# Performance work log

Hardware: AMD Instinct MI355X
Metric: run time of the kernel (lower is better)

The kernel has to match this reference:

```python
import jax, jax.numpy as jnp
import numpy as np

EPS = 1e-6

D_MODEL = 1024
D_STATE = 16
D_CONV = 4
BATCH = 2
SEQ = 2048
D_INNER = 2 * D_MODEL
DT_RANK = D_MODEL // 16
D_FF = 4 * D_MODEL


def rmsnorm(x, w):
    return x * w * jax.lax.rsqrt(jnp.mean(x * x, axis=-1, keepdims=True) + EPS)


def setup_inputs() -> dict:
    key = jax.random.key(0)
    ks = jax.random.split(key, 12)
    s = lambda k, shape, scale=0.02: (jax.random.normal(k, shape, jnp.float32) * scale)
    # S4D-real style A init: A_log[d, n] = log(n+1)
    A_log = jnp.log(jnp.broadcast_to(jnp.arange(1, D_STATE + 1, dtype=jnp.float32), (D_INNER, D_STATE)))
    return {
        "x": jax.random.normal(ks[0], (BATCH, SEQ, D_MODEL), jnp.float32),
        "norm1_w": jnp.ones((D_MODEL,), jnp.float32),
        "norm2_w": jnp.ones((D_MODEL,), jnp.float32),
        "in_proj_w": s(ks[1], (2 * D_INNER, D_MODEL)),
        "conv_w": s(ks[2], (D_INNER, 1, D_CONV), 0.2),
        "conv_b": jnp.zeros((D_INNER,), jnp.float32),
        "x_proj_w": s(ks[3], (DT_RANK + 2 * D_STATE, D_INNER)),
        "dt_proj_w": s(ks[4], (D_INNER, DT_RANK), 0.1),
        "dt_proj_b": jax.random.uniform(ks[5], (D_INNER,), jnp.float32, -4.0, -3.0),
        "A_log": A_log,
        "D": jnp.ones((D_INNER,), jnp.float32),
        "out_proj_w": s(ks[6], (D_MODEL, D_INNER)),
        "w1": s(ks[7], (D_FF, D_MODEL)),
        "w3": s(ks[8], (D_FF, D_MODEL)),
        "w2": s(ks[9], (D_MODEL, D_FF)),
    }


def _ssm(h, in_proj_w, conv_w, conv_b, x_proj_w, dt_proj_w, dt_proj_b, A_log, D, out_proj_w):
    d_inner, d_state = A_log.shape
    dt_rank = dt_proj_w.shape[1]
    d_conv = conv_w.shape[-1]
    bsz = h.shape[0]

    xz = jnp.einsum('bld,ed->ble', h, in_proj_w)          # (B, L, 2*d_inner)
    xin, z = jnp.split(xz, 2, axis=-1)

    # causal depthwise conv over time
    xc = jnp.swapaxes(xin, 1, 2)                           # (B, d_inner, L)
    xc = jax.lax.conv_general_dilated(xc, conv_w, (1,), [(d_conv - 1, 0)],
                                      feature_group_count=d_inner)
    xin = jax.nn.silu(jnp.swapaxes(xc + conv_b[:, None], 1, 2))  # (B, L, d_inner)

    x_dbl = jnp.einsum('bld,ed->ble', xin, x_proj_w)       # (B, L, dt_rank + 2*d_state)
    dt, Bm, Cm = jnp.split(x_dbl, [dt_rank, dt_rank + d_state], axis=-1)
    delta = jax.nn.softplus(jnp.einsum('blr,dr->bld', dt, dt_proj_w) + dt_proj_b)
    A = -jnp.exp(A_log)                                    # (d_inner, d_state)

    def step(hstate, t):
        delta_t, B_t, C_t, x_t = t                         # (B,d), (B,n), (B,n), (B,d)
        dA = jnp.exp(delta_t[..., None] * A)               # (B, d_inner, d_state)
        dBx = (delta_t * x_t)[..., None] * B_t[:, None, :]
        hstate = dA * hstate + dBx
        y = jnp.einsum('bdn,bn->bd', hstate, C_t)
        return hstate, y

    tm = lambda a: jnp.swapaxes(a, 0, 1)                   # time-major
    h0 = jnp.zeros((bsz, d_inner, d_state), h.dtype)
    _, ys = jax.lax.scan(step, h0, (tm(delta), tm(Bm), tm(Cm), tm(xin)))
    y = jnp.swapaxes(ys, 0, 1) + xin * D                   # (B, L, d_inner)
    return jnp.einsum('bld,ed->ble', y * jax.nn.silu(z), out_proj_w)


def reference(x, norm1_w, norm2_w, in_proj_w, conv_w, conv_b, x_proj_w,
              dt_proj_w, dt_proj_b, A_log, D, out_proj_w, w1, w3, w2):
    x = x + _ssm(rmsnorm(x, norm1_w), in_proj_w, conv_w, conv_b, x_proj_w,
                 dt_proj_w, dt_proj_b, A_log, D, out_proj_w)
    h = rmsnorm(x, norm2_w)
    mlp = jnp.einsum('blf,df->bld',
                     jax.nn.silu(jnp.einsum('bld,fd->blf', h, w1)) * jnp.einsum('bld,fd->blf', h, w3),
                     w2)
    return x + mlp
```

## Files before the change

kernel.cpp:

```cpp
#include <hip/hip_runtime.h>

#define DEV __device__ __forceinline__

typedef unsigned short u16;
typedef float f32x4 __attribute__((ext_vector_type(4)));
typedef __bf16 bf16x8 __attribute__((ext_vector_type(8)));

#define CHUNK 64
#define NCH 32

DEV u16 f2b(float f) {
    unsigned u = __builtin_bit_cast(unsigned, f);
    u += 0x7fffu + ((u >> 16) & 1u);
    return (u16)(u >> 16);
}
DEV float b2f(u16 h) { return __builtin_bit_cast(float, (unsigned)h << 16); }
DEV float silu_(float v) { return v / (1.f + __expf(-v)); }
DEV float b2f_lo(unsigned w) { return __builtin_bit_cast(float, w << 16); }
DEV float b2f_hi(unsigned w) { return __builtin_bit_cast(float, w & 0xffff0000u); }
DEV void unpack8(uint4 w, float* f) {
    f[0] = b2f_lo(w.x); f[1] = b2f_hi(w.x);
    f[2] = b2f_lo(w.y); f[3] = b2f_hi(w.y);
    f[4] = b2f_lo(w.z); f[5] = b2f_hi(w.z);
    f[6] = b2f_lo(w.w); f[7] = b2f_hi(w.w);
}

DEV void gload16(const void* g, void* l) {
    __builtin_amdgcn_global_load_lds((const __attribute__((address_space(1))) unsigned int*)g,
                                     (__attribute__((address_space(3))) unsigned int*)l,
                                     16, 0, 0);
}

__global__ __launch_bounds__(256) void cvt_bf16_k(const float* __restrict__ in,
                                                  u16* __restrict__ out, int n4) {
    int i = blockIdx.x * 256 + threadIdx.x;
    if (i >= n4) return;
    float4 v = reinterpret_cast<const float4*>(in)[i];
    ushort4 o;
    o.x = f2b(v.x); o.y = f2b(v.y); o.z = f2b(v.z); o.w = f2b(v.w);
    reinterpret_cast<ushort4*>(out)[i] = o;
}

__global__ __launch_bounds__(256) void rmsnorm_k(const float* __restrict__ x,
                                                 const float* __restrict__ w,
                                                 u16* __restrict__ out) {
    int row = blockIdx.x;
    int t = threadIdx.x;
    float4 v = reinterpret_cast<const float4*>(x + (size_t)row * 1024)[t];
    float s = v.x * v.x + v.y * v.y + v.z * v.z + v.w * v.w;
#pragma unroll
    for (int off = 32; off; off >>= 1) s += __shfl_xor(s, off);
    __shared__ float red[4];
    if ((t & 63) == 0) red[t >> 6] = s;
    __syncthreads();
    float tot = red[0] + red[1] + red[2] + red[3];
    float scale = rsqrtf(tot * (1.f / 1024.f) + 1e-6f);
    float4 wv = reinterpret_cast<const float4*>(w)[t];
    ushort4 o;
    o.x = f2b(v.x * wv.x * scale);
    o.y = f2b(v.y * wv.y * scale);
    o.z = f2b(v.z * wv.z * scale);
    o.w = f2b(v.w * wv.w * scale);
    reinterpret_cast<ushort4*>(out + (size_t)row * 1024)[t] = o;
}

template <int EPI>
__global__ __launch_bounds__(256) void gemm_bt(
    const u16* __restrict__ A, int lda,
    const u16* __restrict__ B, int ldb,
    void* C, int ldc,
    int N, int K,
    const float* __restrict__ bias,
    const void* aux, int ldaux) {
    __shared__ u16 lsA[128 * 32];
    __shared__ u16 lsB[128 * 32];
    const int t = threadIdx.x;
    const int l = t & 63, w = t >> 6;
    const int m0 = blockIdx.x * 128, n0 = blockIdx.y * 128;
    const int wm = w >> 1, wn = w & 1;
    const int lrow = l & 15, lk8 = (l >> 4) * 8;

    const int sr = w * 16 + (l >> 2);
    const int sc = (l & 3) * 8;
    const u16* gA0 = A + (size_t)(m0 + sr) * lda + sc;
    const u16* gA1 = gA0 + (size_t)64 * lda;
    int nr0 = n0 + sr;      if (nr0 > N - 1) nr0 = N - 1;
    int nr1 = n0 + 64 + sr; if (nr1 > N - 1) nr1 = N - 1;
    const u16* gB0 = B + (size_t)nr0 * ldb + sc;
    const u16* gB1 = B + (size_t)nr1 * ldb + sc;
    u16* ldsA0 = &lsA[w * 512];
    u16* ldsA1 = &lsA[2048 + w * 512];
    u16* ldsB0 = &lsB[w * 512];
    u16* ldsB1 = &lsB[2048 + w * 512];

    f32x4 acc[4][4];
#pragma unroll
    for (int i = 0; i < 4; ++i)
#pragma unroll
        for (int j = 0; j < 4; ++j) acc[i][j] = (f32x4){0.f, 0.f, 0.f, 0.f};

    for (int k0 = 0; k0 < K; k0 += 32) {
        gload16(gA0 + k0, ldsA0);
        gload16(gA1 + k0, ldsA1);
        gload16(gB0 + k0, ldsB0);
        gload16(gB1 + k0, ldsB1);
        __syncthreads();
        bf16x8 af[4], bfr[4];
#pragma unroll
        for (int i = 0; i < 4; ++i)
            af[i] = *reinterpret_cast<const bf16x8*>(&lsA[(wm * 64 + i * 16 + lrow) * 32 + lk8]);
#pragma unroll
        for (int j = 0; j < 4; ++j)
            bfr[j] = *reinterpret_cast<const bf16x8*>(&lsB[(wn * 64 + j * 16 + lrow) * 32 + lk8]);
#pragma unroll
        for (int i = 0; i < 4; ++i)
#pragma unroll
            for (int j = 0; j < 4; ++j)
                acc[i][j] = __builtin_amdgcn_mfma_f32_16x16x32_bf16(af[i], bfr[j], acc[i][j], 0, 0, 0);
        __syncthreads();
    }

    const int rbase = m0 + wm * 64 + (l >> 4) * 4;
    const int cbase = n0 + wn * 64 + (l & 15);
#pragma unroll
    for (int i = 0; i < 4; ++i) {
#pragma unroll
        for (int j = 0; j < 4; ++j) {
            int col = cbase + j * 16;
            if (col >= N) continue;
#pragma unroll
            for (int r = 0; r < 4; ++r) {
                int row = rbase + i * 16 + r;
                float v = acc[i][j][r];
                size_t idx = (size_t)row * ldc + col;
                if constexpr (EPI == 0) {
                    ((u16*)C)[idx] = f2b(v);
                } else if constexpr (EPI == 1) {
                    float z = v + bias[col];
                    float sp = z > 20.f ? z : log1pf(__expf(z));
                    ((u16*)C)[idx] = f2b(sp);
                } else if constexpr (EPI == 2) {
                    ((float*)C)[idx] = v + ((const float*)aux)[(size_t)row * ldaux + col];
                } else if constexpr (EPI == 4) {
                    float g = b2f(((const u16*)aux)[(size_t)row * ldaux + col]);
                    ((u16*)C)[idx] = f2b(silu_(g) * v);
                }
            }
        }
    }
}

__global__ __launch_bounds__(256) void conv_k(const u16* __restrict__ xraw,
                                              const float* __restrict__ cw,
                                              const float* __restrict__ cb,
                                              u16* __restrict__ xin) {
    size_t idx = (size_t)blockIdx.x * 256 + threadIdx.x;
    if (idx >= (size_t)4096 * 2048) return;
    int d = (int)(idx & 2047);
    int m = (int)(idx >> 11);
    int lpos = m & 2047, b = m >> 11;
    float acc = cb[d];
#pragma unroll
    for (int j = 0; j < 4; ++j) {
        int lj = lpos - 3 + j;
        if (lj >= 0)
            acc += b2f(xraw[((size_t)(b * 2048 + lj) << 11) + d]) * cw[d * 4 + j];
    }
    xin[idx] = f2b(silu_(acc));
}

__global__ __launch_bounds__(256) void scan_p1(const u16* __restrict__ dlt,
                                               const u16* __restrict__ xin,
                                               const u16* __restrict__ xdbl,
                                               const float* __restrict__ A_log,
                                               float* __restrict__ hfin,
                                               float* __restrict__ sdlt) {
    int blk = blockIdx.x;
    int g = blk & 7, c = (blk >> 3) & 31, b = blk >> 8;
    int d = g * 256 + threadIdx.x;
    __shared__ u16 bc[CHUNK * 32];
    {
        int i = threadIdx.x;
        int r = i >> 2, q = i & 3;
        const u16* src = xdbl + ((size_t)(b * 2048 + c * CHUNK + r) * 96 + 64 + q * 8);
        *reinterpret_cast<uint4*>(&bc[r * 32 + q * 8]) = *reinterpret_cast<const uint4*>(src);
    }
    __syncthreads();
    float A2[16];
#pragma unroll
    for (int n = 0; n < 16; ++n) A2[n] = -__expf(A_log[d * 16 + n]) * 1.44269504f;
    float h[16];
#pragma unroll
    for (int n = 0; n < 16; ++n) h[n] = 0.f;
    float S = 0.f;
    size_t base = ((size_t)(b * 2048 + c * CHUNK) << 11) + d;
#pragma unroll 4
    for (int t = 0; t < CHUNK; ++t) {
        float dl = b2f(dlt[base + ((size_t)t << 11)]);
        float xv = b2f(xin[base + ((size_t)t << 11)]);
        S += dl;
        float dx = dl * xv;
        float Bv[16];
        unpack8(*reinterpret_cast<const uint4*>(&bc[t * 32]), Bv);
        unpack8(*reinterpret_cast<const uint4*>(&bc[t * 32 + 8]), Bv + 8);
#pragma unroll
        for (int n = 0; n < 16; ++n)
            h[n] = __builtin_amdgcn_exp2f(dl * A2[n]) * h[n] + dx * Bv[n];
    }
    float* hf = hfin + ((size_t)((b * NCH + c) * 2048 + d) << 4);
#pragma unroll
    for (int n = 0; n < 4; ++n)
        reinterpret_cast<float4*>(hf)[n] = (float4){h[4*n], h[4*n+1], h[4*n+2], h[4*n+3]};
    sdlt[(b * NCH + c) * 2048 + d] = S;
}

__global__ __launch_bounds__(256) void scan_p2(const float* __restrict__ hfin,
                                               const float* __restrict__ sdlt,
                                               const float* __restrict__ A_log,
                                               float* __restrict__ hini) {
    int t = blockIdx.x * 256 + threadIdx.x;
    int n = t & 15, d = (t >> 4) & 2047, b = t >> 15;
    float A2 = -__expf(A_log[d * 16 + n]) * 1.44269504f;
    float h = 0.f;
    for (int c = 0; c < NCH; ++c) {
        size_t idx = ((size_t)((b * NCH + c) * 2048 + d) << 4) + n;
        hini[idx] = h;
        float P = __builtin_amdgcn_exp2f(A2 * sdlt[(b * NCH + c) * 2048 + d]);
        h = P * h + hfin[idx];
    }
}

__global__ __launch_bounds__(256) void scan_p3(const u16* __restrict__ dlt,
                                               const u16* __restrict__ xin,
                                               const u16* __restrict__ xdbl,
                                               const u16* __restrict__ zb,
                                               const float* __restrict__ A_log,
                                               const float* __restrict__ Dv,
                                               const float* __restrict__ hini,
                                               u16* __restrict__ y2) {
    int blk = blockIdx.x;
    int g = blk & 7, c = (blk >> 3) & 31, b = blk >> 8;
    int d = g * 256 + threadIdx.x;
    __shared__ u16 bc[CHUNK * 32];
    {
        int i = threadIdx.x;
        int r = i >> 2, q = i & 3;
        const u16* src = xdbl + ((size_t)(b * 2048 + c * CHUNK + r) * 96 + 64 + q * 8);
        *reinterpret_cast<uint4*>(&bc[r * 32 + q * 8]) = *reinterpret_cast<const uint4*>(src);
    }
    __syncthreads();
    float A2[16];
#pragma unroll
    for (int n = 0; n < 16; ++n) A2[n] = -__expf(A_log[d * 16 + n]) * 1.44269504f;
    float h[16];
    const float* hi = hini + ((size_t)((b * NCH + c) * 2048 + d) << 4);
#pragma unroll
    for (int n = 0; n < 4; ++n) {
        float4 v = reinterpret_cast<const float4*>(hi)[n];
        h[4*n] = v.x; h[4*n+1] = v.y; h[4*n+2] = v.z; h[4*n+3] = v.w;
    }
    float Dd = Dv[d];
    size_t base = ((size_t)(b * 2048 + c * CHUNK) << 11) + d;
#pragma unroll 4
    for (int t = 0; t < CHUNK; ++t) {
        float dl = b2f(dlt[base + ((size_t)t << 11)]);
        float xv = b2f(xin[base + ((size_t)t << 11)]);
        float zv = b2f(zb[base + ((size_t)t << 11)]);
        float dx = dl * xv;
        float Bv[16], Cv[16];
        unpack8(*reinterpret_cast<const uint4*>(&bc[t * 32]), Bv);
        unpack8(*reinterpret_cast<const uint4*>(&bc[t * 32 + 8]), Bv + 8);
        unpack8(*reinterpret_cast<const uint4*>(&bc[t * 32 + 16]), Cv);
        unpack8(*reinterpret_cast<const uint4*>(&bc[t * 32 + 24]), Cv + 8);
        float y = 0.f;
#pragma unroll
        for (int n = 0; n < 16; ++n) {
            h[n] = __builtin_amdgcn_exp2f(dl * A2[n]) * h[n] + dx * Bv[n];
            y += h[n] * Cv[n];
        }
        y = (y + xv * Dd) * silu_(zv);
        y2[base + ((size_t)t << 11)] = f2b(y);
    }
}


extern "C" void kernel_launch(void* const* d_in, const int* in_sizes, int n_in,
                              void* d_out, int out_size, void* d_ws, size_t ws_size,
                              hipStream_t stream) {
    const float* x         = (const float*)d_in[0];
    const float* n1w       = (const float*)d_in[1];
    const float* n2w       = (const float*)d_in[2];
    const float* w_inproj  = (const float*)d_in[3];
    const float* conv_w    = (const float*)d_in[4];
    const float* conv_b    = (const float*)d_in[5];
    const float* x_projw   = (const float*)d_in[6];
    const float* w_dtproj  = (const float*)d_in[7];
    const float* dt_b      = (const float*)d_in[8];
    const float* A_log     = (const float*)d_in[9];
    const float* Dv        = (const float*)d_in[10];
    const float* w_outproj = (const float*)d_in[11];
    const float* w1        = (const float*)d_in[12];
    const float* w3        = (const float*)d_in[13];
    const float* w2        = (const float*)d_in[14];

    char* ws = (char*)d_ws;
    u16* wbuf    = (u16*)(ws + 0);
    u16* h_bf    = (u16*)(ws + 8388608);
    u16* xraw_bf = (u16*)(ws + 16777216);
    u16* z_bf    = (u16*)(ws + 33554432);
    u16* xin_bf  = (u16*)(ws + 50331648);
    u16* dlt_bf  = (u16*)(ws + 67108864);
    u16* xdbl_bf = (u16*)(ws + 83886080);
    float* sdlt  = (float*)(ws + 84672512);
    float* hfin  = (float*)wbuf;
    float* hini  = (float*)h_bf;
    u16* y2_bf   = xraw_bf;
    float* x2_f  = (float*)(ws + 67108864);
    u16* g1_bf   = xraw_bf;
    u16* act_bf  = g1_bf;

    auto cvt = [&](const float* src, int n) {
        int n4 = n >> 2;
        cvt_bf16_k<<<(n4 + 255) / 256, 256, 0, stream>>>(src, wbuf, n4);
    };

    rmsnorm_k<<<4096, 256, 0, stream>>>(x, n1w, h_bf);
    cvt(w_inproj, 4096 * 1024);
    gemm_bt<0><<<dim3(32, 16), 256, 0, stream>>>(h_bf, 1024, wbuf, 1024, xraw_bf, 2048,
                                                 2048, 1024, nullptr, nullptr, 0);
    gemm_bt<0><<<dim3(32, 16), 256, 0, stream>>>(h_bf, 1024, wbuf + (size_t)2048 * 1024, 1024,
                                                 z_bf, 2048, 2048, 1024, nullptr, nullptr, 0);
    conv_k<<<32768, 256, 0, stream>>>(xraw_bf, conv_w, conv_b, xin_bf);
    cvt(x_projw, 96 * 2048);
    gemm_bt<0><<<dim3(32, 1), 256, 0, stream>>>(xin_bf, 2048, wbuf, 2048, xdbl_bf, 96,
                                                96, 2048, nullptr, nullptr, 0);
    cvt(w_dtproj, 2048 * 64);
    gemm_bt<1><<<dim3(32, 16), 256, 0, stream>>>(xdbl_bf, 96, wbuf, 64, dlt_bf, 2048,
                                                 2048, 64, dt_b, nullptr, 0);
    scan_p1<<<512, 256, 0, stream>>>(dlt_bf, xin_bf, xdbl_bf, A_log, hfin, sdlt);
    scan_p2<<<256, 256, 0, stream>>>(hfin, sdlt, A_log, hini);
    scan_p3<<<512, 256, 0, stream>>>(dlt_bf, xin_bf, xdbl_bf, z_bf, A_log, Dv, hini, y2_bf);
    cvt(w_outproj, 1024 * 2048);
    gemm_bt<2><<<dim3(32, 8), 256, 0, stream>>>(y2_bf, 2048, wbuf, 2048, x2_f, 1024,
                                                1024, 2048, nullptr, x, 1024);
    rmsnorm_k<<<4096, 256, 0, stream>>>(x2_f, n2w, h_bf);
    cvt(w1, 4096 * 1024);
    gemm_bt<0><<<dim3(32, 32), 256, 0, stream>>>(h_bf, 1024, wbuf, 1024, g1_bf, 4096,
                                                 4096, 1024, nullptr, nullptr, 0);
    cvt(w3, 4096 * 1024);
    gemm_bt<4><<<dim3(32, 32), 256, 0, stream>>>(h_bf, 1024, wbuf, 1024, act_bf, 4096,
                                                 4096, 1024, nullptr, g1_bf, 4096);
    cvt(w2, 1024 * 4096);
    gemm_bt<2><<<dim3(32, 8), 256, 0, stream>>>(act_bf, 4096, wbuf, 4096, (float*)d_out, 1024,
                                                1024, 4096, nullptr, x2_f, 1024);
}
```

Before: 751.0 us.

## Split-K the narrow GEMMs, merge in_proj halves, and swizzle workgroup order

The out_proj and w2 GEMMs, which launch only 256 workgroups, now split K in two across blockIdx.z. Each half writes bf16 partials, and a new elementwise kernel adds the two partials to the fp32 residual. The two in_proj GEMMs become one 32x32 launch whose epilogue routes columns to the x or z buffers. Workgroup IDs are also remapped in groups of 8, presumably to spread tiles across XCDs. The intent is more parallelism on the 256 compute units and fewer launches, at the cost of extra partial-sum traffic, an extra reduction kernel, and bf16 rounding of the partial sums.

```diff
diff --git a/kernel.cpp b/kernel.cpp
--- a/kernel.cpp
+++ b/kernel.cpp
@@ -39,6 +39,23 @@
     ushort4 o;
     o.x = f2b(v.x); o.y = f2b(v.y); o.z = f2b(v.z); o.w = f2b(v.w);
     reinterpret_cast<ushort4*>(out)[i] = o;
+}
+
+__global__ __launch_bounds__(256) void addred_k(const float* __restrict__ resid,
+                                                const u16* __restrict__ p0,
+                                                const u16* __restrict__ p1,
+                                                float* __restrict__ out, int n4) {
+    int i = blockIdx.x * 256 + threadIdx.x;
+    if (i >= n4) return;
+    float4 rv = reinterpret_cast<const float4*>(resid)[i];
+    ushort4 a = reinterpret_cast<const ushort4*>(p0)[i];
+    ushort4 b = reinterpret_cast<const ushort4*>(p1)[i];
+    float4 o;
+    o.x = rv.x + b2f(a.x) + b2f(b.x);
+    o.y = rv.y + b2f(a.y) + b2f(b.y);
+    o.z = rv.z + b2f(a.z) + b2f(b.z);
+    o.w = rv.w + b2f(a.w) + b2f(b.w);
+    reinterpret_cast<float4*>(out)[i] = o;
 }
 
 __global__ __launch_bounds__(256) void rmsnorm_k(const float* __restrict__ x,
@@ -64,7 +81,7 @@
     reinterpret_cast<ushort4*>(out + (size_t)row * 1024)[t] = o;
 }
 
-template <int EPI>
+template <int EPI, bool SPLIT = false>
 __global__ __launch_bounds__(256) void gemm_bt(
     const u16* __restrict__ A, int lda,
     const u16* __restrict__ B, int ldb,
@@ -76,18 +93,27 @@
     __shared__ u16 lsB[128 * 32];
     const int t = threadIdx.x;
     const int l = t & 63, w = t >> 6;
-    const int m0 = blockIdx.x * 128, n0 = blockIdx.y * 128;
+
+    int nwg = gridDim.x * gridDim.y;
+    int bid = blockIdx.y * gridDim.x + blockIdx.x;
+    int cpx = nwg >> 3;
+    int swz = (bid & 7) * cpx + (bid >> 3);
+    const int m0 = (swz % gridDim.x) * 128, n0 = (swz / gridDim.x) * 128;
+
+    int klo = 0, klen = K;
+    if constexpr (SPLIT) { klen = K >> 1; klo = blockIdx.z * klen; }
+
     const int wm = w >> 1, wn = w & 1;
     const int lrow = l & 15, lk8 = (l >> 4) * 8;
 
     const int sr = w * 16 + (l >> 2);
     const int sc = (l & 3) * 8;
-    const u16* gA0 = A + (size_t)(m0 + sr) * lda + sc;
+    const u16* gA0 = A + (size_t)(m0 + sr) * lda + sc + klo;
     const u16* gA1 = gA0 + (size_t)64 * lda;
     int nr0 = n0 + sr;      if (nr0 > N - 1) nr0 = N - 1;
     int nr1 = n0 + 64 + sr; if (nr1 > N - 1) nr1 = N - 1;
-    const u16* gB0 = B + (size_t)nr0 * ldb + sc;
-    const u16* gB1 = B + (size_t)nr1 * ldb + sc;
+    const u16* gB0 = B + (size_t)nr0 * ldb + sc + klo;
+    const u16* gB1 = B + (size_t)nr1 * ldb + sc + klo;
     u16* ldsA0 = &lsA[w * 512];
     u16* ldsA1 = &lsA[2048 + w * 512];
     u16* ldsB0 = &lsB[w * 512];
@@ -99,7 +125,7 @@
 #pragma unroll
         for (int j = 0; j < 4; ++j) acc[i][j] = (f32x4){0.f, 0.f, 0.f, 0.f};
 
-    for (int k0 = 0; k0 < K; k0 += 32) {
+    for (int k0 = 0; k0 < klen; k0 += 32) {
         gload16(gA0 + k0, ldsA0);
         gload16(gA1 + k0, ldsA1);
         gload16(gB0 + k0, ldsB0);
@@ -120,6 +146,10 @@
         __syncthreads();
     }
 
+    u16* Cp = (u16*)C;
+    if constexpr (SPLIT)
+        Cp += (size_t)blockIdx.z * gridDim.x * 128 * ldc;
+
     const int rbase = m0 + wm * 64 + (l >> 4) * 4;
     const int cbase = n0 + wn * 64 + (l & 15);
 #pragma unroll
@@ -134,16 +164,21 @@
                 float v = acc[i][j][r];
                 size_t idx = (size_t)row * ldc + col;
                 if constexpr (EPI == 0) {
-                    ((u16*)C)[idx] = f2b(v);
+                    Cp[idx] = f2b(v);
                 } else if constexpr (EPI == 1) {
                     float z = v + bias[col];
                     float sp = z > 20.f ? z : log1pf(__expf(z));
-                    ((u16*)C)[idx] = f2b(sp);
+                    Cp[idx] = f2b(sp);
                 } else if constexpr (EPI == 2) {
                     ((float*)C)[idx] = v + ((const float*)aux)[(size_t)row * ldaux + col];
                 } else if constexpr (EPI == 4) {
                     float g = b2f(((const u16*)aux)[(size_t)row * ldaux + col]);
-                    ((u16*)C)[idx] = f2b(silu_(g) * v);
+                    Cp[idx] = f2b(silu_(g) * v);
+                } else if constexpr (EPI == 5) {
+                    if (col < 2048)
+                        ((u16*)C)[(size_t)row * ldc + col] = f2b(v);
+                    else
+                        ((u16*)aux)[(size_t)row * ldaux + (col - 2048)] = f2b(v);
                 }
             }
         }
@@ -282,7 +317,6 @@
         y2[base + ((size_t)t << 11)] = f2b(y);
     }
 }
-
 
 extern "C" void kernel_launch(void* const* d_in, const int* in_sizes, int n_in,
                               void* d_out, int out_size, void* d_ws, size_t ws_size,
@@ -318,6 +352,9 @@
     float* x2_f  = (float*)(ws + 67108864);
     u16* g1_bf   = xraw_bf;
     u16* act_bf  = g1_bf;
+    u16* pOP     = z_bf;
+    u16* pW2     = xin_bf;
+    const size_t PSTRIDE = (size_t)4096 * 1024;
 
     auto cvt = [&](const float* src, int n) {
         int n4 = n >> 2;
@@ -326,10 +363,8 @@
 
     rmsnorm_k<<<4096, 256, 0, stream>>>(x, n1w, h_bf);
     cvt(w_inproj, 4096 * 1024);
-    gemm_bt<0><<<dim3(32, 16), 256, 0, stream>>>(h_bf, 1024, wbuf, 1024, xraw_bf, 2048,
-                                                 2048, 1024, nullptr, nullptr, 0);
-    gemm_bt<0><<<dim3(32, 16), 256, 0, stream>>>(h_bf, 1024, wbuf + (size_t)2048 * 1024, 1024,
-                                                 z_bf, 2048, 2048, 1024, nullptr, nullptr, 0);
+    gemm_bt<5><<<dim3(32, 32), 256, 0, stream>>>(h_bf, 1024, wbuf, 1024, xraw_bf, 2048,
+                                                 4096, 1024, nullptr, z_bf, 2048);
     conv_k<<<32768, 256, 0, stream>>>(xraw_bf, conv_w, conv_b, xin_bf);
     cvt(x_projw, 96 * 2048);
     gemm_bt<0><<<dim3(32, 1), 256, 0, stream>>>(xin_bf, 2048, wbuf, 2048, xdbl_bf, 96,
@@ -341,8 +376,9 @@
     scan_p2<<<256, 256, 0, stream>>>(hfin, sdlt, A_log, hini);
     scan_p3<<<512, 256, 0, stream>>>(dlt_bf, xin_bf, xdbl_bf, z_bf, A_log, Dv, hini, y2_bf);
     cvt(w_outproj, 1024 * 2048);
-    gemm_bt<2><<<dim3(32, 8), 256, 0, stream>>>(y2_bf, 2048, wbuf, 2048, x2_f, 1024,
-                                                1024, 2048, nullptr, x, 1024);
+    gemm_bt<0, true><<<dim3(32, 8, 2), 256, 0, stream>>>(y2_bf, 2048, wbuf, 2048, pOP, 1024,
+                                                         1024, 2048, nullptr, nullptr, 0);
+    addred_k<<<4096, 256, 0, stream>>>(x, pOP, pOP + PSTRIDE, x2_f, 4096 * 1024 / 4);
     rmsnorm_k<<<4096, 256, 0, stream>>>(x2_f, n2w, h_bf);
     cvt(w1, 4096 * 1024);
     gemm_bt<0><<<dim3(32, 32), 256, 0, stream>>>(h_bf, 1024, wbuf, 1024, g1_bf, 4096,
@@ -351,6 +387,7 @@
     gemm_bt<4><<<dim3(32, 32), 256, 0, stream>>>(h_bf, 1024, wbuf, 1024, act_bf, 4096,
                                                  4096, 1024, nullptr, g1_bf, 4096);
     cvt(w2, 1024 * 4096);
-    gemm_bt<2><<<dim3(32, 8), 256, 0, stream>>>(act_bf, 4096, wbuf, 4096, (float*)d_out, 1024,
-                                                1024, 4096, nullptr, x2_f, 1024);
-}
+    gemm_bt<0, true><<<dim3(32, 8, 2), 256, 0, stream>>>(act_bf, 4096, wbuf, 4096, pW2, 1024,
+                                                         1024, 4096, nullptr, nullptr, 0);
+    addred_k<<<4096, 256, 0, stream>>>(x2_f, pW2, pW2 + PSTRIDE, (float*)d_out, 4096 * 1024 / 4);
+}
```

New measurement: 705.8 us. 1.06x faster.
